# Performance work log

Measured on AMD Instinct MI355X. Metric: run time of the kernel, lower is better.

The kernel has to match this reference:

```python
import jax, jax.numpy as jnp
import numpy as np

EPS = 1e-06        # normalize eps and log eps (module's self.eps)
PDIST_EPS = 1e-06  # torch.nn.PairwiseDistance default eps: ||x1 - x2 + eps||_2

A, C, F = 4096, 8, 64


def setup_inputs() -> dict:
    key = jax.random.key(0)
    x = jax.random.normal(key, (A, C, F), dtype=jnp.float32)
    return {"x": x}


def reference(x) -> jnp.ndarray:
    a = x.shape[0]
    c = x.shape[1]
    # F.normalize(p=2, dim=-1, eps=EPS): x / max(||x||_2, eps)
    nrm = jnp.linalg.norm(x, axis=-1, keepdims=True)
    xn = x / jnp.maximum(nrm, EPS)
    # pairwise cosine similarity per group: [C, A, A]
    sim = jnp.einsum('acf,bcf->cab', xn, xn)
    # mask self-similarity on the diagonal with -1
    diag = jnp.eye(a, dtype=bool)[None, :, :]
    sim = jnp.where(diag, -1.0, sim)
    # nearest neighbor per (c, a): argmax over b -> [C, A] -> [A, C]
    idx = jnp.argmax(sim, axis=-1).T
    # gather matched embeddings: x_match[a, c, f] = xn[idx[a, c], c, f]
    x_match = xn[idx, jnp.arange(c)[None, :], :]
    # PairwiseDistance(p=2, eps=1e-6): ||x - x_match + eps||_2 over last dim
    min_dist = jnp.linalg.norm(xn - x_match + PDIST_EPS, axis=-1)
    loss = -jnp.mean(jnp.log(min_dist + EPS))
    return loss
```

## Files before the change

kernel.cpp:

```cpp
#include <hip/hip_runtime.h>
#include <math.h>

#define AN 4096
#define CN 8
#define FN 64
#define ACN (AN*CN)
#define NSEG 4
#define ITERS 8

typedef __attribute__((ext_vector_type(8))) short bf16x8;
typedef __attribute__((ext_vector_type(4))) float f32x4;

#define GLL16(gsrc, ldst) \
    __builtin_amdgcn_global_load_lds( \
        (const __attribute__((address_space(1))) void*)(gsrc), \
        (__attribute__((address_space(3))) void*)(ldst), 16, 0, 0)

__device__ inline unsigned short f2bf(float f) {
    unsigned u = __float_as_uint(f);
    unsigned r = ((u >> 16) & 1) + 0x7FFFu;
    return (unsigned short)((u + r) >> 16);
}

__global__ __launch_bounds__(256) void k1_normalize(const float* __restrict__ x,
                                                    unsigned short* __restrict__ xnb,
                                                    float* __restrict__ inv)
{
    int tid  = threadIdx.x;
    int grp  = tid >> 4;
    int slot = tid & 15;
    #pragma unroll
    for (int s = 0; s < 4; ++s) {
        int V = blockIdx.x * 64 + s * 16 + grp;
        const float4 v = *(const float4*)(x + (size_t)V * FN + slot * 4);
        float ss = v.x*v.x + v.y*v.y + v.z*v.z + v.w*v.w;
        ss += __shfl_xor(ss, 1);
        ss += __shfl_xor(ss, 2);
        ss += __shfl_xor(ss, 4);
        ss += __shfl_xor(ss, 8);
        float sc = 1.0f / fmaxf(sqrtf(ss), 1e-6f);
        int a = V >> 3, c = V & 7;
        ushort4 ob;
        ob.x = f2bf(v.x * sc); ob.y = f2bf(v.y * sc);
        ob.z = f2bf(v.z * sc); ob.w = f2bf(v.w * sc);
        *(ushort4*)(xnb + ((size_t)c * AN + a) * FN + slot * 4) = ob;
        if (slot == 0) inv[V] = sc;
    }
}

__global__ __launch_bounds__(256, 2) void k2_argmax(const unsigned short* __restrict__ xnb,
                                                    unsigned int* __restrict__ pP)
{
    __shared__ char ldsc[5 * 16384];

    int blk  = blockIdx.x;
    int seg  = blk & (NSEG - 1);
    int rt   = (blk >> 2) & 31;
    int c    = blk >> 7;
    int a0   = rt * 128;
    int col0 = seg * 1024;

    const char* __restrict__ Xc = (const char*)(xnb + (size_t)c * AN * FN);

    int tid  = threadIdx.x;
    int lane = tid & 63;
    int w    = tid >> 6;
    int l15  = lane & 15;
    int quad = lane >> 4;
    int srow = lane >> 3;
    int sslot = lane & 7;

    int gl_lane = srow * 128 + ((sslot ^ srow) << 4);
    const char* gA = Xc + (size_t)(a0 + w * 32) * 128 + gl_lane;
    const char* gB = Xc + (size_t)(col0 + w * 32) * 128 + gl_lane;
    char* ldsA = ldsc + w * 4096;
    char* ldsB = ldsc + 16384 + w * 4096;

    GLL16(gA,        ldsA);
    GLL16(gA + 1024, ldsA + 1024);
    GLL16(gA + 2048, ldsA + 2048);
    GLL16(gA + 3072, ldsA + 3072);
    __syncthreads();

    int ab0 = l15 * 128 + ((quad ^ (l15 & 7)) << 4);
    int ab1 = ab0 ^ 64;
    bf16x8 afr[8][2];
    #pragma unroll
    for (int mi = 0; mi < 8; ++mi) {
        afr[mi][0] = *(const bf16x8*)(ldsc + ab0 + mi * 2048);
        afr[mi][1] = *(const bf16x8*)(ldsc + ab1 + mi * 2048);
    }

    int rb0 = 16384 + (w * 32 + l15) * 128 + ((quad ^ (l15 & 7)) << 4);
    int rb1 = rb0 ^ 64;

    float bestp[32];
    #pragma unroll
    for (int i = 0; i < 32; ++i) bestp[i] = 0.0f;

    const f32x4 two = {2.0f, 2.0f, 2.0f, 2.0f};

#define STAGE_B(IT) do { \
        const char* _g = gB + (size_t)(IT) * 16384; \
        char* _l = ldsB + ((IT) & 3) * 16384; \
        GLL16(_g,        _l); \
        GLL16(_g + 1024, _l + 1024); \
        GLL16(_g + 2048, _l + 2048); \
        GLL16(_g + 3072, _l + 3072); \
    } while (0)

    STAGE_B(0);
    STAGE_B(1);
    STAGE_B(2);

    #pragma unroll
    for (int it = 0; it < ITERS; ++it) {
        if (it <= ITERS - 4) STAGE_B(it + 3);

        if (it <= ITERS - 4)      { asm volatile("s_waitcnt vmcnt(12)" ::: "memory"); }
        else if (it == ITERS - 3) { asm volatile("s_waitcnt vmcnt(8)"  ::: "memory"); }
        else if (it == ITERS - 2) { asm volatile("s_waitcnt vmcnt(4)"  ::: "memory"); }
        else                      { asm volatile("s_waitcnt vmcnt(0)"  ::: "memory"); }

        const int bo = (it & 3) * 16384;

        f32x4 acc[8][2];
        #pragma unroll
        for (int ks = 0; ks < 2; ++ks) {
            #pragma unroll
            for (int ni = 0; ni < 2; ++ni) {
                bf16x8 bfr = *(const bf16x8*)(ldsc + (ks ? rb1 : rb0) + bo + ni * 2048);
                #pragma unroll
                for (int mi = 0; mi < 8; ++mi)
                    acc[mi][ni] = __builtin_amdgcn_mfma_f32_16x16x32_bf16(
                        afr[mi][ks], bfr, (ks == 0) ? two : acc[mi][ni], 0, 0, 0);
            }
        }

        int colblk = col0 + it * 128 + w * 32;
        #pragma unroll
        for (int mi = 0; mi < 8; ++mi) {
            int rfrag = a0 + mi * 16;
            #pragma unroll
            for (int r = 0; r < 4; ++r) {
                unsigned p0 = (__float_as_uint(acc[mi][0][r]) & 0xFFFFF000u)
                            | (unsigned)(colblk + l15);
                unsigned p1 = (__float_as_uint(acc[mi][1][r]) & 0xFFFFF000u)
                            | (unsigned)(colblk + 16 + l15);
                float c0 = __uint_as_float(p0);
                float c1 = __uint_as_float(p1);
                if (rfrag == colblk)      { if (l15 == quad * 4 + r) c0 = 0.0f; }
                if (rfrag == colblk + 16) { if (l15 == quad * 4 + r) c1 = 0.0f; }
                int bi = mi * 4 + r;
                bestp[bi] = fmaxf(fmaxf(c0, c1), bestp[bi]);
            }
        }
    }
#undef STAGE_B

    #pragma unroll
    for (int i = 0; i < 32; ++i) {
        float v = bestp[i];
        v = fmaxf(v, __shfl_xor(v, 1));
        v = fmaxf(v, __shfl_xor(v, 2));
        v = fmaxf(v, __shfl_xor(v, 4));
        v = fmaxf(v, __shfl_xor(v, 8));
        bestp[i] = v;
    }
    __syncthreads();
    float* red = (float*)ldsc;
    if (l15 == 0) {
        #pragma unroll
        for (int mi = 0; mi < 8; ++mi)
            #pragma unroll
            for (int r = 0; r < 4; ++r)
                red[w * 128 + mi * 16 + quad * 4 + r] = bestp[mi * 4 + r];
    }
    __syncthreads();
    if (tid < 128) {
        float p = fmaxf(fmaxf(red[tid], red[128 + tid]),
                        fmaxf(red[256 + tid], red[384 + tid]));
        int a = a0 + tid;
        pP[(size_t)seg * ACN + (size_t)a * CN + c] = __float_as_uint(p);
    }
}

__global__ __launch_bounds__(256) void k3_dist(const float* __restrict__ x,
                                               const float* __restrict__ inv,
                                               const unsigned int* __restrict__ pP,
                                               float* __restrict__ partials)
{
    int tid = threadIdx.x;
    int id = blockIdx.x * 256 + tid;
    float p0 = __uint_as_float(pP[id]);
    float p1 = __uint_as_float(pP[ACN + id]);
    float p2 = __uint_as_float(pP[2 * ACN + id]);
    float p3 = __uint_as_float(pP[3 * ACN + id]);
    unsigned pm = __float_as_uint(fmaxf(fmaxf(p0, p1), fmaxf(p2, p3)));
    int m = (int)(pm & 0xFFFu);
    int c = id & 7;
    int idb = m * CN + c;
    float sa = inv[id];
    float sb = inv[idb];
    const float* xa = x + (size_t)id  * FN;
    const float* xb = x + (size_t)idb * FN;
    float ss = 0.0f;
    #pragma unroll
    for (int q = 0; q < 16; ++q) {
        float4 va = *(const float4*)(xa + 4 * q);
        float4 vb = *(const float4*)(xb + 4 * q);
        float d0 = va.x * sa - vb.x * sb + 1e-6f;
        float d1 = va.y * sa - vb.y * sb + 1e-6f;
        float d2 = va.z * sa - vb.z * sb + 1e-6f;
        float d3 = va.w * sa - vb.w * sb + 1e-6f;
        ss += d0*d0 + d1*d1 + d2*d2 + d3*d3;
    }
    float val = logf(sqrtf(ss) + 1e-6f);

    float t = val;
    #pragma unroll
    for (int off = 32; off > 0; off >>= 1) t += __shfl_down(t, off);
    __shared__ float ws4[4];
    if ((tid & 63) == 0) ws4[tid >> 6] = t;
    __syncthreads();
    if (tid == 0)
        partials[blockIdx.x] = ws4[0] + ws4[1] + ws4[2] + ws4[3];
}

__global__ __launch_bounds__(64) void k4_final(const float* __restrict__ partials,
                                               float* __restrict__ out)
{
    int t = threadIdx.x;
    float v = partials[t] + partials[t + 64];
    #pragma unroll
    for (int off = 32; off > 0; off >>= 1) v += __shfl_down(v, off);
    if (t == 0) out[0] = -v / (float)ACN;
}

extern "C" void kernel_launch(void* const* d_in, const int* in_sizes, int n_in,
                              void* d_out, int out_size, void* d_ws, size_t ws_size,
                              hipStream_t stream)
{
    const float* x = (const float*)d_in[0];
    unsigned short* xnb = (unsigned short*)d_ws;
    float* inv = (float*)(xnb + (size_t)AN * CN * FN);
    unsigned int* pP = (unsigned int*)(inv + ACN);
    float* partials = (float*)(pP + NSEG * ACN);

    k1_normalize<<<512, 256, 0, stream>>>(x, xnb, inv);
    k2_argmax  <<<CN * 32 * NSEG, 256, 0, stream>>>(xnb, pP);
    k3_dist    <<<128, 256, 0, stream>>>(x, inv, pP, partials);
    k4_final   <<<1, 64, 0, stream>>>(partials, (float*)d_out);
}
```

Measured before the change: 95.52 us.

## Retile argmax kernel into 2x2 wave grid with double-buffered B for higher occupancy

Each workgroup's four waves now form a 2x2 grid. Each wave covers 64 rows by 32 columns instead of 128 rows by 32 columns, with 64-column B tiles over twice as many iterations. The four-deep B ring with explicit vmcnt waits becomes a two-buffer scheme guarded by a barrier each iteration. LDS drops from 80KB to 32KB and per-thread accumulators and fragments are halved, which allows four workgroups per CU instead of two to better hide latency. The cost is a workgroup barrier per iteration, a shallower prefetch pipeline, and less A-fragment reuse per B load.

```diff
diff --git a/kernel.cpp b/kernel.cpp
--- a/kernel.cpp
+++ b/kernel.cpp
@@ -6,7 +6,7 @@
 #define FN 64
 #define ACN (AN*CN)
 #define NSEG 4
-#define ITERS 8
+#define ITERS 16
 
 typedef __attribute__((ext_vector_type(8))) short bf16x8;
 typedef __attribute__((ext_vector_type(4))) float f32x4;
@@ -48,10 +48,10 @@
     }
 }
 
-__global__ __launch_bounds__(256, 2) void k2_argmax(const unsigned short* __restrict__ xnb,
+__global__ __launch_bounds__(256, 4) void k2_argmax(const unsigned short* __restrict__ xnb,
                                                     unsigned int* __restrict__ pP)
 {
-    __shared__ char ldsc[5 * 16384];
+    __shared__ char ldsc[32768];
 
     int blk  = blockIdx.x;
     int seg  = blk & (NSEG - 1);
@@ -65,82 +65,74 @@
     int tid  = threadIdx.x;
     int lane = tid & 63;
     int w    = tid >> 6;
+    int wr   = w >> 1;
+    int wc   = w & 1;
     int l15  = lane & 15;
     int quad = lane >> 4;
     int srow = lane >> 3;
     int sslot = lane & 7;
 
     int gl_lane = srow * 128 + ((sslot ^ srow) << 4);
+
     const char* gA = Xc + (size_t)(a0 + w * 32) * 128 + gl_lane;
-    const char* gB = Xc + (size_t)(col0 + w * 32) * 128 + gl_lane;
     char* ldsA = ldsc + w * 4096;
-    char* ldsB = ldsc + 16384 + w * 4096;
-
     GLL16(gA,        ldsA);
     GLL16(gA + 1024, ldsA + 1024);
     GLL16(gA + 2048, ldsA + 2048);
     GLL16(gA + 3072, ldsA + 3072);
-    __syncthreads();
-
-    int ab0 = l15 * 128 + ((quad ^ (l15 & 7)) << 4);
+
+    const char* gB = Xc + (size_t)col0 * 128 + (size_t)w * 1024 + gl_lane;
+#define STAGE_B(T) do { \
+        const char* _g = gB + (size_t)(T) * 8192; \
+        char* _l = ldsc + 16384 + ((T) & 1) * 8192 + w * 1024; \
+        GLL16(_g,        _l); \
+        GLL16(_g + 4096, _l + 4096); \
+    } while (0)
+
+    STAGE_B(0);
+    __syncthreads();
+
+    int ab0 = (wr * 64 + l15) * 128 + ((quad ^ (l15 & 7)) << 4);
     int ab1 = ab0 ^ 64;
-    bf16x8 afr[8][2];
-    #pragma unroll
-    for (int mi = 0; mi < 8; ++mi) {
+    bf16x8 afr[4][2];
+    #pragma unroll
+    for (int mi = 0; mi < 4; ++mi) {
         afr[mi][0] = *(const bf16x8*)(ldsc + ab0 + mi * 2048);
         afr[mi][1] = *(const bf16x8*)(ldsc + ab1 + mi * 2048);
     }
 
-    int rb0 = 16384 + (w * 32 + l15) * 128 + ((quad ^ (l15 & 7)) << 4);
+    int rb0 = 16384 + (wc * 32 + l15) * 128 + ((quad ^ (l15 & 7)) << 4);
     int rb1 = rb0 ^ 64;
 
-    float bestp[32];
-    #pragma unroll
-    for (int i = 0; i < 32; ++i) bestp[i] = 0.0f;
+    float bestp[16];
+    #pragma unroll
+    for (int i = 0; i < 16; ++i) bestp[i] = 0.0f;
 
     const f32x4 two = {2.0f, 2.0f, 2.0f, 2.0f};
 
-#define STAGE_B(IT) do { \
-        const char* _g = gB + (size_t)(IT) * 16384; \
-        char* _l = ldsB + ((IT) & 3) * 16384; \
-        GLL16(_g,        _l); \
-        GLL16(_g + 1024, _l + 1024); \
-        GLL16(_g + 2048, _l + 2048); \
-        GLL16(_g + 3072, _l + 3072); \
-    } while (0)
-
-    STAGE_B(0);
-    STAGE_B(1);
-    STAGE_B(2);
-
     #pragma unroll
     for (int it = 0; it < ITERS; ++it) {
-        if (it <= ITERS - 4) STAGE_B(it + 3);
-
-        if (it <= ITERS - 4)      { asm volatile("s_waitcnt vmcnt(12)" ::: "memory"); }
-        else if (it == ITERS - 3) { asm volatile("s_waitcnt vmcnt(8)"  ::: "memory"); }
-        else if (it == ITERS - 2) { asm volatile("s_waitcnt vmcnt(4)"  ::: "memory"); }
-        else                      { asm volatile("s_waitcnt vmcnt(0)"  ::: "memory"); }
-
-        const int bo = (it & 3) * 16384;
-
-        f32x4 acc[8][2];
+        if (it < ITERS - 1) STAGE_B(it + 1);
+
+        const int bo = (it & 1) * 8192;
+
+        f32x4 acc[4][2];
         #pragma unroll
         for (int ks = 0; ks < 2; ++ks) {
             #pragma unroll
             for (int ni = 0; ni < 2; ++ni) {
                 bf16x8 bfr = *(const bf16x8*)(ldsc + (ks ? rb1 : rb0) + bo + ni * 2048);
                 #pragma unroll
-                for (int mi = 0; mi < 8; ++mi)
+                for (int mi = 0; mi < 4; ++mi)
                     acc[mi][ni] = __builtin_amdgcn_mfma_f32_16x16x32_bf16(
                         afr[mi][ks], bfr, (ks == 0) ? two : acc[mi][ni], 0, 0, 0);
             }
         }
 
-        int colblk = col0 + it * 128 + w * 32;
+        int colblk = col0 + it * 64 + wc * 32;
         #pragma unroll
-        for (int mi = 0; mi < 8; ++mi) {
-            int rfrag = a0 + mi * 16;
+        for (int mi = 0; mi < 4; ++mi) {
+            int rfrag = a0 + wr * 64 + mi * 16;
             #pragma unroll
             for (int r = 0; r < 4; ++r) {
                 unsigned p0 = (__float_as_uint(acc[mi][0][r]) & 0xFFFFF000u)
@@ -155,11 +147,13 @@
                 bestp[bi] = fmaxf(fmaxf(c0, c1), bestp[bi]);
             }
         }
+
+        __syncthreads();
     }
 #undef STAGE_B
 
     #pragma unroll
-    for (int i = 0; i < 32; ++i) {
+    for (int i = 0; i < 16; ++i) {
         float v = bestp[i];
         v = fmaxf(v, __shfl_xor(v, 1));
         v = fmaxf(v, __shfl_xor(v, 2));
@@ -171,15 +165,15 @@
     float* red = (float*)ldsc;
     if (l15 == 0) {
         #pragma unroll
-        for (int mi = 0; mi < 8; ++mi)
+        for (int mi = 0; mi < 4; ++mi)
             #pragma unroll
             for (int r = 0; r < 4; ++r)
-                red[w * 128 + mi * 16 + quad * 4 + r] = bestp[mi * 4 + r];
+                red[w * 64 + mi * 16 + quad * 4 + r] = bestp[mi * 4 + r];
     }
     __syncthreads();
     if (tid < 128) {
-        float p = fmaxf(fmaxf(red[tid], red[128 + tid]),
-                        fmaxf(red[256 + tid], red[384 + tid]));
+        int wr2 = tid >> 6, r64 = tid & 63;
+        float p = fmaxf(red[(2 * wr2) * 64 + r64], red[(2 * wr2 + 1) * 64 + r64]);
         int a = a0 + tid;
         pP[(size_t)seg * ACN + (size_t)a * CN + c] = __float_as_uint(p);
     }
```

Result: no change. 95.75 us (+0.2%).
